# Kernel optimization log

Hardware: AMD Instinct MI355X
Metric: run time of the kernel (lower is better)

## Reference

```python
import jax, jax.numpy as jnp
import numpy as np

B, N, H = 32, 512, 128
LN_EPS = 1e-5

def _layernorm(x):
    # LayerNorm over last dim, no affine (elementwise_affine=False)
    mu = jnp.mean(x, axis=-1, keepdims=True)
    var = jnp.var(x, axis=-1, keepdims=True)
    return (x - mu) * jax.lax.rsqrt(var + LN_EPS)

def setup_inputs() -> dict:
    key = jax.random.key(0)
    k0, k1, k2, k3 = jax.random.split(key, 4)
    s = jax.random.normal(k0, (B, N, H), dtype=jnp.float32)
    ev = jax.random.normal(k1, (B, N, N, 3), dtype=jnp.float32)
    mask = (jax.random.uniform(k2, (B, N, N, 1)) > 0.5).astype(jnp.float32)
    W1 = jax.random.normal(k3, (H, H), dtype=jnp.float32) / np.sqrt(H)
    b1 = jnp.zeros((H,), dtype=jnp.float32)
    return {"s": s, "ev": ev, "mask": mask, "W1": W1, "b1": b1}

def reference(s, ev, mask, W1, b1):
    # lin1: Linear -> LayerNorm (no affine) -> SiLU
    h = jnp.einsum('bnh,kh->bnk', s, W1) + b1          # (B, N, H)
    h = jax.nn.silu(_layernorm(h))
    # Fused CFConv: v[b,i,c,d] = sum_j mask[b,i,j] * ev[b,i,j,c] * h[b,j,d]
    mev = ev * mask                                     # (B, N, N, 3)
    v = jnp.einsum('bijc,bjd->bicd', mev, h)            # (B, N, 3, H)
    return v
```

## Files before the change

kernel.cpp:

```cpp
#include <hip/hip_runtime.h>
#include <hip/hip_bf16.h>

#define B_ 32
#define N_ 512
#define H_ 128

typedef float f32x4 __attribute__((ext_vector_type(4)));
typedef short short8 __attribute__((ext_vector_type(8)));
typedef short short4v __attribute__((ext_vector_type(4)));

static __device__ __forceinline__ float bf2f(unsigned short u) {
  union { unsigned int ui; float f; } x;
  x.ui = ((unsigned int)u) << 16;
  return x.f;
}
static __device__ __forceinline__ unsigned short f2bf(float f) {
  __hip_bfloat16 h = __float2bfloat16(f);
  return *reinterpret_cast<unsigned short*>(&h);
}

__global__ __launch_bounds__(256) void lin_ln_silu_kernel(
    const float* __restrict__ s, const float* __restrict__ W1,
    const float* __restrict__ b1, unsigned short* __restrict__ h_t) {
  __shared__ float s_sh[32 * 132];
  __shared__ unsigned short w_sh[128 * 132];
  __shared__ unsigned short ht_sh[128 * 40];
  const int t = threadIdx.x;
  const int b = blockIdx.y;
  const int n0 = blockIdx.x * 32;

#pragma unroll
  for (int r = 0; r < 16; ++r) {
    int q = t + 256 * r;
    int d = q >> 5, part = q & 31;
    float4 v = *reinterpret_cast<const float4*>(W1 + d * H_ + part * 4);
    short4v w;
    w.x = (short)f2bf(v.x); w.y = (short)f2bf(v.y);
    w.z = (short)f2bf(v.z); w.w = (short)f2bf(v.w);
    *reinterpret_cast<short4v*>(&w_sh[d * 132 + part * 4]) = w;
  }
#pragma unroll
  for (int r = 0; r < 4; ++r) {
    int q = t + 256 * r;
    int n = q >> 5, part = q & 31;
    float4 v = *reinterpret_cast<const float4*>(
        s + ((size_t)b * N_ + n0 + n) * H_ + part * 4);
    *reinterpret_cast<float4*>(&s_sh[n * 132 + part * 4]) = v;
  }
  __syncthreads();

  const int a = t & 15;
  const int g = t >> 4;
  float acc[2][8];
#pragma unroll
  for (int nn = 0; nn < 2; ++nn)
#pragma unroll
    for (int dd = 0; dd < 8; ++dd) acc[nn][dd] = 0.f;

  float bias[8];
#pragma unroll
  for (int dd = 0; dd < 8; ++dd) bias[dd] = b1[dd * 16 + a];

  for (int k = 0; k < 128; k += 4) {
    float wf[8][4];
#pragma unroll
    for (int dd = 0; dd < 8; ++dd) {
      short4v wv =
          *reinterpret_cast<const short4v*>(&w_sh[(dd * 16 + a) * 132 + k]);
      wf[dd][0] = bf2f((unsigned short)wv.x);
      wf[dd][1] = bf2f((unsigned short)wv.y);
      wf[dd][2] = bf2f((unsigned short)wv.z);
      wf[dd][3] = bf2f((unsigned short)wv.w);
    }
#pragma unroll
    for (int nn = 0; nn < 2; ++nn) {
      float4 sv =
          *reinterpret_cast<const float4*>(&s_sh[(nn * 16 + g) * 132 + k]);
#pragma unroll
      for (int dd = 0; dd < 8; ++dd) {
        acc[nn][dd] += sv.x * wf[dd][0] + sv.y * wf[dd][1] +
                       sv.z * wf[dd][2] + sv.w * wf[dd][3];
      }
    }
  }

#pragma unroll
  for (int nn = 0; nn < 2; ++nn) {
    float s1 = 0.f, s2 = 0.f;
#pragma unroll
    for (int dd = 0; dd < 8; ++dd) {
      float x = acc[nn][dd] + bias[dd];
      acc[nn][dd] = x;
      s1 += x;
      s2 += x * x;
    }
#pragma unroll
    for (int off = 8; off >= 1; off >>= 1) {
      s1 += __shfl_xor(s1, off);
      s2 += __shfl_xor(s2, off);
    }
    float mean = s1 * (1.f / 128.f);
    float var = s2 * (1.f / 128.f) - mean * mean;
    float rs = rsqrtf(var + 1e-5f);
#pragma unroll
    for (int dd = 0; dd < 8; ++dd) {
      float x = (acc[nn][dd] - mean) * rs;
      float y = x / (1.f + __expf(-x));
      ht_sh[(dd * 16 + a) * 40 + nn * 16 + g] = f2bf(y);
    }
  }
  __syncthreads();

#pragma unroll
  for (int r = 0; r < 2; ++r) {
    int q = t + 256 * r;
    int d = q >> 2, part = q & 3;
    float4 v = *reinterpret_cast<const float4*>(&ht_sh[d * 40 + part * 8]);
    *reinterpret_cast<float4*>(
        h_t + ((size_t)b * 128 + d) * 512 + n0 + part * 8) = v;
  }
}

__global__ __launch_bounds__(256, 1) void cfconv_mfma_kernel(
    const float* __restrict__ ev, const float* __restrict__ mask,
    const unsigned short* __restrict__ h_t, float* __restrict__ out) {
  __shared__ unsigned short hL[128 * 512];
  const int t = threadIdx.x;
  const int b = blockIdx.y;
  const int i0 = blockIdx.x * 64;
  const int w = t >> 6, l = t & 63;
  const int l15 = l & 15, quad = l >> 4;
  const int ig = i0 + w * 16 + l15;

  {
    const unsigned short* hb = h_t + (size_t)b * 65536;
#pragma unroll 4
    for (int r2 = 0; r2 < 32; ++r2) {
      int row = w * 32 + r2;
      float4 v = *reinterpret_cast<const float4*>(hb + row * 512 + l * 8);
      *reinterpret_cast<float4*>(
          &hL[row * 512 + (l >> 3) * 64 + (((l & 7) ^ (row & 7)) * 8)]) = v;
    }
  }
  __syncthreads();

  f32x4 acc[3][8];
#pragma unroll
  for (int mt = 0; mt < 3; ++mt)
#pragma unroll
    for (int nt = 0; nt < 8; ++nt)
#pragma unroll
      for (int e = 0; e < 4; ++e) acc[mt][nt][e] = 0.f;

  const float* evrow =
      ev + ((size_t)(b * N_) + ig) * (N_ * 3) + quad * 24;
  const float* mrow = mask + ((size_t)(b * N_) + ig) * N_ + quad * 8;

  f32x4 evA[12], mkA[4], evB[12], mkB[4];
  short8 av[3][2];

#define ALOADO(DST, PTR, OFF)                                    \
  asm volatile("global_load_dwordx4 %0, %1, off offset:" OFF     \
               : "=v"(DST) : "v"(PTR))

#define ISSUE_SET(EVX, MKX, R)                                   \
  do {                                                           \
    const char* ep_ = (const char*)evrow + (R)*768;              \
    const char* mp_ = (const char*)mrow + (R)*256;               \
    ALOADO(EVX[0], ep_, "0");    ALOADO(EVX[1], ep_, "16");      \
    ALOADO(EVX[2], ep_, "32");   ALOADO(EVX[3], ep_, "48");      \
    ALOADO(EVX[4], ep_, "64");   ALOADO(EVX[5], ep_, "80");      \
    ALOADO(EVX[6], ep_, "384");  ALOADO(EVX[7], ep_, "400");     \
    ALOADO(EVX[8], ep_, "416");  ALOADO(EVX[9], ep_, "432");     \
    ALOADO(EVX[10], ep_, "448"); ALOADO(EVX[11], ep_, "464");    \
    ALOADO(MKX[0], mp_, "0");    ALOADO(MKX[1], mp_, "16");      \
    ALOADO(MKX[2], mp_, "128");  ALOADO(MKX[3], mp_, "144");     \
  } while (0)

#define VMW(n)                                       \
  do {                                               \
    asm volatile("s_waitcnt vmcnt(" #n ")");         \
    __builtin_amdgcn_sched_barrier(0);               \
  } while (0)

#define CONV(EVX, MKX)                                                  \
  do {                                                                  \
    _Pragma("unroll") for (int ks_ = 0; ks_ < 2; ++ks_) {               \
      float p_[8][3];                                                   \
      _Pragma("unroll") for (int e_ = 0; e_ < 8; ++e_) {                \
        float mv_ = MKX[ks_ * 2 + (e_ >> 2)][e_ & 3];                   \
        _Pragma("unroll") for (int c_ = 0; c_ < 3; ++c_) {              \
          int f_ = e_ * 3 + c_;                                         \
          p_[e_][c_] = EVX[ks_ * 6 + (f_ >> 2)][f_ & 3] * mv_;          \
        }                                                               \
      }                                                                 \
      _Pragma("unroll") for (int c_ = 0; c_ < 3; ++c_) {                \
        short8 a_;                                                      \
        _Pragma("unroll") for (int e_ = 0; e_ < 8; ++e_)                \
            a_[e_] = (short)f2bf(p_[e_][c_]);                           \
        av[c_][ks_] = a_;                                               \
      }                                                                 \
    }                                                                   \
  } while (0)

#define COMPUTE(J0)                                                     \
  do {                                                                  \
    _Pragma("unroll") for (int ks_ = 0; ks_ < 2; ++ks_) {               \
      _Pragma("unroll") for (int nt_ = 0; nt_ < 8; ++nt_) {             \
        int d_ = nt_ * 16 + l15;                                        \
        short8 bv_ = *reinterpret_cast<const short8*>(                  \
            &hL[d_ * 512 + (J0) +                                       \
                (((ks_ * 4 + quad) ^ (l15 & 7)) * 8)]);                 \
        _Pragma("unroll") for (int mt_ = 0; mt_ < 3; ++mt_)             \
            acc[mt_][nt_] = __builtin_amdgcn_mfma_f32_16x16x32_bf16(    \
                av[mt_][ks_], bv_, acc[mt_][nt_], 0, 0, 0);             \
      }                                                                 \
    }                                                                   \
  } while (0)

  ISSUE_SET(evA, mkA, 0);
  ISSUE_SET(evB, mkB, 1);

  VMW(16); CONV(evA, mkA); ISSUE_SET(evA, mkA, 2); COMPUTE(0);
  VMW(16); CONV(evB, mkB); ISSUE_SET(evB, mkB, 3); COMPUTE(64);
  VMW(16); CONV(evA, mkA); ISSUE_SET(evA, mkA, 4); COMPUTE(128);
  VMW(16); CONV(evB, mkB); ISSUE_SET(evB, mkB, 5); COMPUTE(192);
  VMW(16); CONV(evA, mkA); ISSUE_SET(evA, mkA, 6); COMPUTE(256);
  VMW(16); CONV(evB, mkB); ISSUE_SET(evB, mkB, 7); COMPUTE(320);
  VMW(16); CONV(evA, mkA); COMPUTE(384);
  VMW(0);  CONV(evB, mkB); COMPUTE(448);

#undef COMPUTE
#undef CONV
#undef VMW
#undef ISSUE_SET
#undef ALOADO

  __syncthreads();
  {
    float* zf = reinterpret_cast<float*>(hL) + w * 6144;
#pragma unroll
    for (int c = 0; c < 3; ++c)
#pragma unroll
      for (int nt = 0; nt < 8; ++nt)
#pragma unroll
        for (int r = 0; r < 4; ++r)
          zf[((quad * 4 + r) * 3 + c) * 128 + nt * 16 + l15] = acc[c][nt][r];
    asm volatile("s_waitcnt lgkmcnt(0)");
    __builtin_amdgcn_sched_barrier(0);
    float* ob = out + ((size_t)(b * N_) + i0 + w * 16) * 3 * 128;
#pragma unroll
    for (int k = 0; k < 24; ++k) {
      int flat = k * 256 + l * 4;
      f32x4 v = *reinterpret_cast<const f32x4*>(zf + flat);
      *reinterpret_cast<f32x4*>(ob + flat) = v;
    }
  }
}

extern "C" void kernel_launch(void* const* d_in, const int* in_sizes, int n_in,
                              void* d_out, int out_size, void* d_ws,
                              size_t ws_size, hipStream_t stream) {
  const float* s = (const float*)d_in[0];
  const float* ev = (const float*)d_in[1];
  const float* mask = (const float*)d_in[2];
  const float* W1 = (const float*)d_in[3];
  const float* b1 = (const float*)d_in[4];
  float* out = (float*)d_out;
  unsigned short* h_t = (unsigned short*)d_ws;

  lin_ln_silu_kernel<<<dim3(N_ / 32, B_), 256, 0, stream>>>(s, W1, b1, h_t);
  cfconv_mfma_kernel<<<dim3(N_ / 64, B_), 256, 0, stream>>>(ev, mask, h_t, out);
}
```

Before: 213.9 us.

## Compute lin1 GEMM with bf16 MFMA and cross-wave LayerNorm reduction

Replaces the scalar FMA GEMM in the linear+LayerNorm+SiLU kernel with 16x16x32 bf16 MFMA instructions. Inputs s are now converted to bf16 in shared memory, and each wave owns 32 output columns. The LayerNorm row statistics are therefore reduced across four waves through a small shared buffer and an extra barrier. Launch bounds also request 2 blocks per CU. This kernel is likely a small part of the total time next to the CFConv kernel, and converting s to bf16 adds a little extra precision loss.

```diff
diff --git a/kernel.cpp b/kernel.cpp
--- a/kernel.cpp
+++ b/kernel.cpp
@@ -19,25 +19,28 @@
   return *reinterpret_cast<unsigned short*>(&h);
 }
 
-__global__ __launch_bounds__(256) void lin_ln_silu_kernel(
+__global__ __launch_bounds__(256, 2) void lin_ln_silu_kernel(
     const float* __restrict__ s, const float* __restrict__ W1,
     const float* __restrict__ b1, unsigned short* __restrict__ h_t) {
-  __shared__ float s_sh[32 * 132];
-  __shared__ unsigned short w_sh[128 * 132];
+  __shared__ unsigned short sA[32 * 136];
+  __shared__ unsigned short wB[128 * 136];
   __shared__ unsigned short ht_sh[128 * 40];
+  __shared__ float buf[4][32][2];
   const int t = threadIdx.x;
   const int b = blockIdx.y;
   const int n0 = blockIdx.x * 32;
+  const int w = t >> 6, l = t & 63;
+  const int l15 = l & 15, quad = l >> 4;
 
 #pragma unroll
   for (int r = 0; r < 16; ++r) {
     int q = t + 256 * r;
     int d = q >> 5, part = q & 31;
     float4 v = *reinterpret_cast<const float4*>(W1 + d * H_ + part * 4);
-    short4v w;
-    w.x = (short)f2bf(v.x); w.y = (short)f2bf(v.y);
-    w.z = (short)f2bf(v.z); w.w = (short)f2bf(v.w);
-    *reinterpret_cast<short4v*>(&w_sh[d * 132 + part * 4]) = w;
+    short4v wv;
+    wv.x = (short)f2bf(v.x); wv.y = (short)f2bf(v.y);
+    wv.z = (short)f2bf(v.z); wv.w = (short)f2bf(v.w);
+    *reinterpret_cast<short4v*>(&wB[d * 136 + part * 4]) = wv;
   }
 #pragma unroll
   for (int r = 0; r < 4; ++r) {
@@ -45,70 +48,98 @@
     int n = q >> 5, part = q & 31;
     float4 v = *reinterpret_cast<const float4*>(
         s + ((size_t)b * N_ + n0 + n) * H_ + part * 4);
-    *reinterpret_cast<float4*>(&s_sh[n * 132 + part * 4]) = v;
-  }
-  __syncthreads();
-
-  const int a = t & 15;
-  const int g = t >> 4;
-  float acc[2][8];
-#pragma unroll
-  for (int nn = 0; nn < 2; ++nn)
-#pragma unroll
-    for (int dd = 0; dd < 8; ++dd) acc[nn][dd] = 0.f;
-
-  float bias[8];
-#pragma unroll
-  for (int dd = 0; dd < 8; ++dd) bias[dd] = b1[dd * 16 + a];
-
-  for (int k = 0; k < 128; k += 4) {
-    float wf[8][4];
-#pragma unroll
-    for (int dd = 0; dd < 8; ++dd) {
-      short4v wv =
-          *reinterpret_cast<const short4v*>(&w_sh[(dd * 16 + a) * 132 + k]);
-      wf[dd][0] = bf2f((unsigned short)wv.x);
-      wf[dd][1] = bf2f((unsigned short)wv.y);
-      wf[dd][2] = bf2f((unsigned short)wv.z);
-      wf[dd][3] = bf2f((unsigned short)wv.w);
+    short4v sv;
+    sv.x = (short)f2bf(v.x); sv.y = (short)f2bf(v.y);
+    sv.z = (short)f2bf(v.z); sv.w = (short)f2bf(v.w);
+    *reinterpret_cast<short4v*>(&sA[n * 136 + part * 4]) = sv;
+  }
+  __syncthreads();
+
+  f32x4 acc[2][2];
+#pragma unroll
+  for (int mt = 0; mt < 2; ++mt)
+#pragma unroll
+    for (int ct = 0; ct < 2; ++ct)
+#pragma unroll
+      for (int e = 0; e < 4; ++e) acc[mt][ct][e] = 0.f;
+
+#pragma unroll
+  for (int ks = 0; ks < 4; ++ks) {
+    short8 av[2], bv[2];
+#pragma unroll
+    for (int mt = 0; mt < 2; ++mt)
+      av[mt] = *reinterpret_cast<const short8*>(
+          &sA[(mt * 16 + l15) * 136 + ks * 32 + quad * 8]);
+#pragma unroll
+    for (int ct = 0; ct < 2; ++ct)
+      bv[ct] = *reinterpret_cast<const short8*>(
+          &wB[(w * 32 + ct * 16 + l15) * 136 + ks * 32 + quad * 8]);
+#pragma unroll
+    for (int mt = 0; mt < 2; ++mt)
+#pragma unroll
+      for (int ct = 0; ct < 2; ++ct)
+        acc[mt][ct] = __builtin_amdgcn_mfma_f32_16x16x32_bf16(
+            av[mt], bv[ct], acc[mt][ct], 0, 0, 0);
+  }
+
+  const float bb[2] = {b1[w * 32 + l15], b1[w * 32 + 16 + l15]};
+#pragma unroll
+  for (int mt = 0; mt < 2; ++mt)
+#pragma unroll
+    for (int ct = 0; ct < 2; ++ct)
+#pragma unroll
+      for (int e = 0; e < 4; ++e) acc[mt][ct][e] += bb[ct];
+
+  float s1[2][4], s2[2][4];
+#pragma unroll
+  for (int mt = 0; mt < 2; ++mt)
+#pragma unroll
+    for (int r = 0; r < 4; ++r) {
+      float x0 = acc[mt][0][r], x1 = acc[mt][1][r];
+      s1[mt][r] = x0 + x1;
+      s2[mt][r] = x0 * x0 + x1 * x1;
     }
 #pragma unroll
-    for (int nn = 0; nn < 2; ++nn) {
-      float4 sv =
-          *reinterpret_cast<const float4*>(&s_sh[(nn * 16 + g) * 132 + k]);
-#pragma unroll
-      for (int dd = 0; dd < 8; ++dd) {
-        acc[nn][dd] += sv.x * wf[dd][0] + sv.y * wf[dd][1] +
-                       sv.z * wf[dd][2] + sv.w * wf[dd][3];
+  for (int off = 1; off <= 8; off <<= 1) {
+#pragma unroll
+    for (int mt = 0; mt < 2; ++mt)
+#pragma unroll
+      for (int r = 0; r < 4; ++r) {
+        s1[mt][r] += __shfl_xor(s1[mt][r], off);
+        s2[mt][r] += __shfl_xor(s2[mt][r], off);
+      }
+  }
+  if (l15 == 0) {
+#pragma unroll
+    for (int mt = 0; mt < 2; ++mt)
+#pragma unroll
+      for (int r = 0; r < 4; ++r) {
+        int row = mt * 16 + quad * 4 + r;
+        buf[w][row][0] = s1[mt][r];
+        buf[w][row][1] = s2[mt][r];
+      }
+  }
+  __syncthreads();
+
+#pragma unroll
+  for (int mt = 0; mt < 2; ++mt)
+#pragma unroll
+    for (int r = 0; r < 4; ++r) {
+      int row = mt * 16 + quad * 4 + r;
+      float S1 = buf[0][row][0] + buf[1][row][0] + buf[2][row][0] +
+                 buf[3][row][0];
+      float S2 = buf[0][row][1] + buf[1][row][1] + buf[2][row][1] +
+                 buf[3][row][1];
+      float mean = S1 * (1.f / 128.f);
+      float var = S2 * (1.f / 128.f) - mean * mean;
+      float rs = rsqrtf(var + 1e-5f);
+#pragma unroll
+      for (int ct = 0; ct < 2; ++ct) {
+        float x = (acc[mt][ct][r] - mean) * rs;
+        float y = x / (1.f + __expf(-x));
+        ht_sh[(w * 32 + ct * 16 + l15) * 40 + row] = f2bf(y);
       }
     }
-  }
-
-#pragma unroll
-  for (int nn = 0; nn < 2; ++nn) {
-    float s1 = 0.f, s2 = 0.f;
-#pragma unroll
-    for (int dd = 0; dd < 8; ++dd) {
-      float x = acc[nn][dd] + bias[dd];
-      acc[nn][dd] = x;
-      s1 += x;
-      s2 += x * x;
-    }
-#pragma unroll
-    for (int off = 8; off >= 1; off >>= 1) {
-      s1 += __shfl_xor(s1, off);
-      s2 += __shfl_xor(s2, off);
-    }
-    float mean = s1 * (1.f / 128.f);
-    float var = s2 * (1.f / 128.f) - mean * mean;
-    float rs = rsqrtf(var + 1e-5f);
-#pragma unroll
-    for (int dd = 0; dd < 8; ++dd) {
-      float x = (acc[nn][dd] - mean) * rs;
-      float y = x / (1.f + __expf(-x));
-      ht_sh[(dd * 16 + a) * 40 + nn * 16 + g] = f2bf(y);
-    }
-  }
   __syncthreads();
 
 #pragma unroll
```

Result: faster. 203.3 us (-5.0%).
